# Performance work log

Hardware: AMD Instinct MI355X
Metric: run time of the kernel (lower is better)

Reference implementation:

```python
import jax, jax.numpy as jnp
import numpy as np

IN_F = 4096
OUT_F = 4096
BATCH = 1024

def setup_inputs() -> dict:
    key = jax.random.key(0)
    k = jax.random.split(key, 7)
    x = jax.random.normal(k[0], (BATCH, IN_F), dtype=jnp.float32)
    weight_mu = jax.random.normal(k[1], (OUT_F, IN_F), dtype=jnp.float32) * (1.0 / np.sqrt(IN_F))
    # torch init: uniform(-5,-3) for sigma params (raw values, used directly as std)
    weight_sigma = jax.random.uniform(k[2], (OUT_F, IN_F), dtype=jnp.float32, minval=-5.0, maxval=-3.0)
    bias_mu = jnp.zeros((OUT_F,), dtype=jnp.float32)
    bias_sigma = jax.random.uniform(k[3], (OUT_F,), dtype=jnp.float32, minval=-5.0, maxval=-3.0)
    eps_w = jax.random.normal(k[4], (OUT_F, IN_F), dtype=jnp.float32)
    eps_b = jax.random.normal(k[5], (OUT_F,), dtype=jnp.float32)
    return {"x": x, "weight_mu": weight_mu, "weight_sigma": weight_sigma,
            "bias_mu": bias_mu, "bias_sigma": bias_sigma,
            "eps_w": eps_w, "eps_b": eps_b}

def reference(x, weight_mu, weight_sigma, bias_mu, bias_sigma, eps_w, eps_b):
    # training-mode forward: reparameterized weight sample then dense matmul
    weight = weight_mu + eps_w * weight_sigma        # [out, in]
    bias = bias_mu + eps_b * bias_sigma              # [out]
    # F.linear(x, W, b) = x @ W.T + b
    return jnp.einsum('bi,oi->bo', x, weight) + bias
```

## Files before the change

kernel.cpp:

```cpp
#include <hip/hip_runtime.h>
#include <hip/hip_bf16.h>
#include <stdint.h>

#define M_BATCH 1024
#define N_OUT   4096
#define K_IN    4096

#define BM 128
#define BN 128
#define KPER   (K_IN / 2)
#define BK2    32
#define KITER2 (KPER / BK2)

typedef __attribute__((ext_vector_type(8))) __bf16 bf16x8_t;
typedef __attribute__((ext_vector_type(4))) float f32x4_t;
typedef __attribute__((ext_vector_type(4))) float fvec4;
typedef __attribute__((ext_vector_type(4))) unsigned short us4_t;

__device__ __forceinline__ unsigned short f2bf_bits(float f) {
    union { __hip_bfloat16 h; unsigned short u; } cvt;
    cvt.h = __float2bfloat16(f);
    return cvt.u;
}

__global__ __launch_bounds__(256) void prep_kernel(
    const float* __restrict__ x,
    const float* __restrict__ wmu,
    const float* __restrict__ wsig,
    const float* __restrict__ epsw,
    unsigned short* __restrict__ wb,
    unsigned short* __restrict__ xb)
{
    const size_t tid = (size_t)blockIdx.x * blockDim.x + threadIdx.x;
    const size_t T   = (size_t)1048576;

    const fvec4* wmu4  = (const fvec4*)wmu;
    const fvec4* wsig4 = (const fvec4*)wsig;
    const fvec4* epsw4 = (const fvec4*)epsw;
    us4_t* wb4 = (us4_t*)wb;

    fvec4 m[4], s[4], e[4];
    #pragma unroll
    for (int r = 0; r < 4; ++r) {
        const size_t i = tid + (size_t)r * T;
        m[r] = __builtin_nontemporal_load(wmu4  + i);
        s[r] = __builtin_nontemporal_load(wsig4 + i);
        e[r] = __builtin_nontemporal_load(epsw4 + i);
    }
    #pragma unroll
    for (int r = 0; r < 4; ++r) {
        us4_t o;
        o.x = f2bf_bits(fmaf(e[r].x, s[r].x, m[r].x));
        o.y = f2bf_bits(fmaf(e[r].y, s[r].y, m[r].y));
        o.z = f2bf_bits(fmaf(e[r].z, s[r].z, m[r].z));
        o.w = f2bf_bits(fmaf(e[r].w, s[r].w, m[r].w));
        wb4[tid + (size_t)r * T] = o;
    }

    fvec4 v = __builtin_nontemporal_load((const fvec4*)x + tid);
    us4_t o;
    o.x = f2bf_bits(v.x);
    o.y = f2bf_bits(v.y);
    o.z = f2bf_bits(v.z);
    o.w = f2bf_bits(v.w);
    ((us4_t*)xb)[tid] = o;
}

__global__ __launch_bounds__(512, 2) void gemm_bt_kernel(
    const unsigned short* __restrict__ A,
    const unsigned short* __restrict__ B,
    const float* __restrict__ bmu,
    const float* __restrict__ bsig,
    const float* __restrict__ ebias,
    float* __restrict__ C)
{
    __shared__ unsigned short lds[4 * 16384];

    const int t   = threadIdx.x;
    const int b   = blockIdx.x;
    const int bn  = (b & 7) | (((b >> 3) & 3) << 3);
    const int bm  = b >> 5;
    const int bm0 = bm * BM;
    const int bn0 = bn * BN;
    const int lane  = t & 63;
    const int wave  = t >> 6;
    const int khalf = wave >> 2;
    const int quadw = wave & 3;
    const int wrow  = (quadw >> 1) * 64;
    const int wcol  = (quadw & 1) * 64;
    const int lm    = lane & 15;
    const int quad  = lane >> 4;
    const int fq    = quad ^ ((lm >> 1) & 3);

    f32x4_t acc[4][4] = {};

    const int row   = t >> 2;
    const int chlog = (t & 3) ^ ((t >> 3) & 3);
    const unsigned short* srcs[4];
    srcs[0] = A + (size_t)(bm0 + row) * K_IN + chlog * 8;
    srcs[1] = srcs[0] + KPER;
    srcs[2] = B + (size_t)(bn0 + row) * K_IN + chlog * 8;
    srcs[3] = srcs[2] + KPER;
    char* dstt = (char*)lds + t * 16;

    auto STAGE = [&](int it) {
        const int koff = it * BK2;
        char* d = dstt + (it & 3) * 32768;
        #pragma unroll
        for (int s = 0; s < 4; ++s)
            __builtin_amdgcn_global_load_lds(
                (const __attribute__((address_space(1))) void*)(srcs[s] + koff),
                (__attribute__((address_space(3))) void*)(d + s * 8192), 16, 0, 0);
    };

    auto COMPUTE = [&](int it) {
        const unsigned short* Lb = lds + (it & 3) * 16384;
        const unsigned short* Ah = Lb + khalf * 4096 + (wrow + lm) * 32 + fq * 8;
        const unsigned short* Bh = Lb + 8192 + khalf * 4096 + (wcol + lm) * 32 + fq * 8;
        bf16x8_t a_frag[4], b_frag[4];
        #pragma unroll
        for (int im = 0; im < 4; im++)
            a_frag[im] = *(const bf16x8_t*)(Ah + im * 512);
        #pragma unroll
        for (int jn = 0; jn < 4; jn++)
            b_frag[jn] = *(const bf16x8_t*)(Bh + jn * 512);
        #pragma unroll
        for (int im = 0; im < 4; im++)
            #pragma unroll
            for (int jn = 0; jn < 4; jn++)
                acc[im][jn] = __builtin_amdgcn_mfma_f32_16x16x32_bf16(
                    a_frag[im], b_frag[jn], acc[im][jn], 0, 0, 0);
        __builtin_amdgcn_sched_barrier(0);
    };

    STAGE(0); STAGE(1); STAGE(2);

    for (int it = 0; it < KITER2 - 3; ++it) {
        asm volatile("s_waitcnt vmcnt(8)\n\ts_barrier" ::: "memory");
        STAGE(it + 3);
        COMPUTE(it);
    }
    asm volatile("s_waitcnt vmcnt(8)\n\ts_barrier" ::: "memory");
    COMPUTE(KITER2 - 3);
    asm volatile("s_waitcnt vmcnt(4)\n\ts_barrier" ::: "memory");
    COMPUTE(KITER2 - 2);
    asm volatile("s_waitcnt vmcnt(0)\n\ts_barrier" ::: "memory");
    COMPUTE(KITER2 - 1);

    f32x4_t* red = (f32x4_t*)lds;
    if (wave >= 4) {
        #pragma unroll
        for (int im = 0; im < 4; im++)
            #pragma unroll
            for (int jn = 0; jn < 4; jn++)
                red[quadw * 1024 + (im * 4 + jn) * 64 + lane] = acc[im][jn];
    }
    __syncthreads();
    if (wave < 4) {
        #pragma unroll
        for (int jn = 0; jn < 4; jn++) {
            const int gn = bn0 + wcol + jn * 16 + lm;
            const float bias = bmu[gn] + ebias[gn] * bsig[gn];
            #pragma unroll
            for (int im = 0; im < 4; im++) {
                const f32x4_t part = red[quadw * 1024 + (im * 4 + jn) * 64 + lane];
                const int gm0 = bm0 + wrow + im * 16 + quad * 4;
                #pragma unroll
                for (int r = 0; r < 4; r++)
                    C[(size_t)(gm0 + r) * N_OUT + gn] = acc[im][jn][r] + part[r] + bias;
            }
        }
    }
}

__global__ __launch_bounds__(256) void naive_kernel(
    const float* __restrict__ x, const float* __restrict__ wmu,
    const float* __restrict__ wsig, const float* __restrict__ bmu,
    const float* __restrict__ bsig, const float* __restrict__ epsw,
    const float* __restrict__ epsb, float* __restrict__ out)
{
    const int o = blockIdx.x * blockDim.x + threadIdx.x;
    const int b = blockIdx.y;
    const float4* xr = (const float4*)(x + (size_t)b * K_IN);
    const float4* mr = (const float4*)(wmu + (size_t)o * K_IN);
    const float4* sr = (const float4*)(wsig + (size_t)o * K_IN);
    const float4* er = (const float4*)(epsw + (size_t)o * K_IN);
    float s = 0.f;
    for (int k = 0; k < K_IN / 4; k++) {
        float4 xv = xr[k], m = mr[k], sg = sr[k], e = er[k];
        s += xv.x * fmaf(e.x, sg.x, m.x);
        s += xv.y * fmaf(e.y, sg.y, m.y);
        s += xv.z * fmaf(e.z, sg.z, m.z);
        s += xv.w * fmaf(e.w, sg.w, m.w);
    }
    out[(size_t)b * N_OUT + o] = s + bmu[o] + epsb[o] * bsig[o];
}

extern "C" void kernel_launch(void* const* d_in, const int* in_sizes, int n_in,
                              void* d_out, int out_size, void* d_ws, size_t ws_size,
                              hipStream_t stream)
{
    const float* x    = (const float*)d_in[0];
    const float* wmu  = (const float*)d_in[1];
    const float* wsig = (const float*)d_in[2];
    const float* bmu  = (const float*)d_in[3];
    const float* bsig = (const float*)d_in[4];
    const float* epsw = (const float*)d_in[5];
    const float* epsb = (const float*)d_in[6];
    float* out = (float*)d_out;

    const size_t need = ((size_t)N_OUT * K_IN + (size_t)M_BATCH * K_IN) * sizeof(unsigned short);
    if (ws_size >= need) {
        unsigned short* wb = (unsigned short*)d_ws;
        unsigned short* xb = wb + (size_t)N_OUT * K_IN;
        prep_kernel<<<4096, 256, 0, stream>>>(x, wmu, wsig, epsw, wb, xb);
        gemm_bt_kernel<<<256, 512, 0, stream>>>(xb, wb, bmu, bsig, epsb, out);
    } else {
        dim3 grid(N_OUT / 256, M_BATCH);
        naive_kernel<<<grid, 256, 0, stream>>>(x, wmu, wsig, bmu, bsig, epsw, epsb, out);
    }
}
```

Measured before the change: 246.1 us.

## Fuse weight/activation prep into GEMM with chunked producer flags

```diff
diff --git a/kernel.cpp b/kernel.cpp
--- a/kernel.cpp
+++ b/kernel.cpp
@@ -8,9 +8,11 @@
 
 #define BM 128
 #define BN 128
-#define KPER   (K_IN / 2)
+#define KPER   2048
 #define BK2    32
-#define KITER2 (KPER / BK2)
+#define NSLAB  64
+#define NCHUNK 16
+#define NFLAG  8
 
 typedef __attribute__((ext_vector_type(8))) __bf16 bf16x8_t;
 typedef __attribute__((ext_vector_type(4))) float f32x4_t;
@@ -23,55 +25,17 @@
     return cvt.u;
 }
 
-__global__ __launch_bounds__(256) void prep_kernel(
+__global__ __launch_bounds__(512, 2) void fused_kernel(
     const float* __restrict__ x,
     const float* __restrict__ wmu,
     const float* __restrict__ wsig,
     const float* __restrict__ epsw,
-    unsigned short* __restrict__ wb,
-    unsigned short* __restrict__ xb)
-{
-    const size_t tid = (size_t)blockIdx.x * blockDim.x + threadIdx.x;
-    const size_t T   = (size_t)1048576;
-
-    const fvec4* wmu4  = (const fvec4*)wmu;
-    const fvec4* wsig4 = (const fvec4*)wsig;
-    const fvec4* epsw4 = (const fvec4*)epsw;
-    us4_t* wb4 = (us4_t*)wb;
-
-    fvec4 m[4], s[4], e[4];
-    #pragma unroll
-    for (int r = 0; r < 4; ++r) {
-        const size_t i = tid + (size_t)r * T;
-        m[r] = __builtin_nontemporal_load(wmu4  + i);
-        s[r] = __builtin_nontemporal_load(wsig4 + i);
-        e[r] = __builtin_nontemporal_load(epsw4 + i);
-    }
-    #pragma unroll
-    for (int r = 0; r < 4; ++r) {
-        us4_t o;
-        o.x = f2bf_bits(fmaf(e[r].x, s[r].x, m[r].x));
-        o.y = f2bf_bits(fmaf(e[r].y, s[r].y, m[r].y));
-        o.z = f2bf_bits(fmaf(e[r].z, s[r].z, m[r].z));
-        o.w = f2bf_bits(fmaf(e[r].w, s[r].w, m[r].w));
-        wb4[tid + (size_t)r * T] = o;
-    }
-
-    fvec4 v = __builtin_nontemporal_load((const fvec4*)x + tid);
-    us4_t o;
-    o.x = f2bf_bits(v.x);
-    o.y = f2bf_bits(v.y);
-    o.z = f2bf_bits(v.z);
-    o.w = f2bf_bits(v.w);
-    ((us4_t*)xb)[tid] = o;
-}
-
-__global__ __launch_bounds__(512, 2) void gemm_bt_kernel(
-    const unsigned short* __restrict__ A,
-    const unsigned short* __restrict__ B,
     const float* __restrict__ bmu,
     const float* __restrict__ bsig,
     const float* __restrict__ ebias,
+    unsigned short* __restrict__ wb,
+    unsigned short* __restrict__ xb,
+    unsigned int*   __restrict__ ready,
     float* __restrict__ C)
 {
     __shared__ unsigned short lds[4 * 16384];
@@ -94,27 +58,62 @@
 
     f32x4_t acc[4][4] = {};
 
-    const int row   = t >> 2;
+    const int prow  = b * 16 + (t >> 5);
+    const int pxrow = b * 4 + (t >> 7);
+    fvec4 pm[2], ps[2], pe[2];
+    float px[2];
+
+    auto PRODUCE_LOAD = [&](int cc) {
+        #pragma unroll
+        for (int h = 0; h < 2; ++h) {
+            const size_t wo = (size_t)prow * K_IN + h * KPER + cc * 128 + ((t & 31) << 2);
+            pm[h] = __builtin_nontemporal_load((const fvec4*)(wmu  + wo));
+            ps[h] = __builtin_nontemporal_load((const fvec4*)(wsig + wo));
+            pe[h] = __builtin_nontemporal_load((const fvec4*)(epsw + wo));
+            const size_t xo = (size_t)pxrow * K_IN + h * KPER + cc * 128 + (t & 127);
+            px[h] = __builtin_nontemporal_load(x + xo);
+        }
+    };
+    auto CONVERT_STORE = [&](int cc) {
+        #pragma unroll
+        for (int h = 0; h < 2; ++h) {
+            us4_t o;
+            o.x = f2bf_bits(fmaf(pe[h].x, ps[h].x, pm[h].x));
+            o.y = f2bf_bits(fmaf(pe[h].y, ps[h].y, pm[h].y));
+            o.z = f2bf_bits(fmaf(pe[h].z, ps[h].z, pm[h].z));
+            o.w = f2bf_bits(fmaf(pe[h].w, ps[h].w, pm[h].w));
+            *(us4_t*)(wb + (size_t)prow * K_IN + h * KPER + cc * 128 + ((t & 31) << 2)) = o;
+            xb[(size_t)pxrow * K_IN + h * KPER + cc * 128 + (t & 127)] = f2bf_bits(px[h]);
+        }
+    };
+    auto POLL = [&](int f) {
+        if (t == 0) {
+            while (__hip_atomic_load(&ready[f], __ATOMIC_RELAXED,
+                                     __HIP_MEMORY_SCOPE_AGENT) < 256u)
+                __builtin_amdgcn_s_sleep(2);
+        }
+    };
+
+    const int grow  = t >> 2;
     const int chlog = (t & 3) ^ ((t >> 3) & 3);
     const unsigned short* srcs[4];
-    srcs[0] = A + (size_t)(bm0 + row) * K_IN + chlog * 8;
+    srcs[0] = xb + (size_t)(bm0 + grow) * K_IN + chlog * 8;
     srcs[1] = srcs[0] + KPER;
-    srcs[2] = B + (size_t)(bn0 + row) * K_IN + chlog * 8;
+    srcs[2] = wb + (size_t)(bn0 + grow) * K_IN + chlog * 8;
     srcs[3] = srcs[2] + KPER;
     char* dstt = (char*)lds + t * 16;
 
-    auto STAGE = [&](int it) {
-        const int koff = it * BK2;
-        char* d = dstt + (it & 3) * 32768;
-        #pragma unroll
-        for (int s = 0; s < 4; ++s)
+    auto STAGE = [&](int s) {
+        const int koff = s * BK2;
+        char* d = dstt + (s & 3) * 32768;
+        #pragma unroll
+        for (int q = 0; q < 4; ++q)
             __builtin_amdgcn_global_load_lds(
-                (const __attribute__((address_space(1))) void*)(srcs[s] + koff),
-                (__attribute__((address_space(3))) void*)(d + s * 8192), 16, 0, 0);
-    };
-
-    auto COMPUTE = [&](int it) {
-        const unsigned short* Lb = lds + (it & 3) * 16384;
+                (const __attribute__((address_space(1))) void*)(srcs[q] + koff),
+                (__attribute__((address_space(3))) void*)(d + q * 8192), 16, 0, 0);
+    };
+    auto COMPUTE = [&](int s) {
+        const unsigned short* Lb = lds + (s & 3) * 16384;
         const unsigned short* Ah = Lb + khalf * 4096 + (wrow + lm) * 32 + fq * 8;
         const unsigned short* Bh = Lb + 8192 + khalf * 4096 + (wcol + lm) * 32 + fq * 8;
         bf16x8_t a_frag[4], b_frag[4];
@@ -133,19 +132,59 @@
         __builtin_amdgcn_sched_barrier(0);
     };
 
-    STAGE(0); STAGE(1); STAGE(2);
-
-    for (int it = 0; it < KITER2 - 3; ++it) {
-        asm volatile("s_waitcnt vmcnt(8)\n\ts_barrier" ::: "memory");
-        STAGE(it + 3);
-        COMPUTE(it);
-    }
-    asm volatile("s_waitcnt vmcnt(8)\n\ts_barrier" ::: "memory");
-    COMPUTE(KITER2 - 3);
-    asm volatile("s_waitcnt vmcnt(4)\n\ts_barrier" ::: "memory");
-    COMPUTE(KITER2 - 2);
-    asm volatile("s_waitcnt vmcnt(0)\n\ts_barrier" ::: "memory");
-    COMPUTE(KITER2 - 1);
+    PRODUCE_LOAD(0);
+
+    for (int c = 0; c < 19; ++c) {
+        if (c < NCHUNK) {
+            CONVERT_STORE(c);
+            if (c + 1 < NCHUNK) PRODUCE_LOAD(c + 1);
+        }
+        if (c < 3) {
+            if (c == 1) {
+                asm volatile("s_waitcnt vmcnt(0)" ::: "memory");
+                __builtin_amdgcn_fence(__ATOMIC_RELEASE, "agent");
+                __builtin_amdgcn_s_barrier();
+                if (t == 0)
+                    __hip_atomic_fetch_add(&ready[0], 1u, __ATOMIC_RELAXED,
+                                           __HIP_MEMORY_SCOPE_AGENT);
+            }
+            continue;
+        }
+        const int s0 = (c - 3) * 4;
+        if (c == 3) {
+            POLL(0);
+            __builtin_amdgcn_s_barrier();
+            STAGE(0); STAGE(1); STAGE(2);
+        } else if (c <= 16) {
+            POLL((4 * c - 6) >> 3);
+        }
+        asm volatile("s_waitcnt vmcnt(8)" ::: "memory");
+        __builtin_amdgcn_s_barrier();
+        if (s0 + 3 < NSLAB) STAGE(s0 + 3);
+        COMPUTE(s0 + 0);
+        asm volatile("s_waitcnt vmcnt(8)" ::: "memory");
+        __builtin_amdgcn_s_barrier();
+        if (s0 + 4 < NSLAB) STAGE(s0 + 4);
+        COMPUTE(s0 + 1);
+        const bool sig = (c & 1) && (c <= 15);
+        if (sig) {
+            asm volatile("s_waitcnt vmcnt(0)" ::: "memory");
+            __builtin_amdgcn_fence(__ATOMIC_RELEASE, "agent");
+        }
+        if (c == 18) asm volatile("s_waitcnt vmcnt(4)" ::: "memory");
+        else         asm volatile("s_waitcnt vmcnt(8)" ::: "memory");
+        __builtin_amdgcn_s_barrier();
+        if (sig && t == 0)
+            __hip_atomic_fetch_add(&ready[c >> 1], 1u, __ATOMIC_RELAXED,
+                                   __HIP_MEMORY_SCOPE_AGENT);
+        if (s0 + 5 < NSLAB) STAGE(s0 + 5);
+        COMPUTE(s0 + 2);
+        if (c == 18) asm volatile("s_waitcnt vmcnt(0)" ::: "memory");
+        else         asm volatile("s_waitcnt vmcnt(8)" ::: "memory");
+        __builtin_amdgcn_s_barrier();
+        if (s0 + 6 < NSLAB) STAGE(s0 + 6);
+        COMPUTE(s0 + 3);
+    }
 
     f32x4_t* red = (f32x4_t*)lds;
     if (wave >= 4) {
@@ -209,12 +248,15 @@
     const float* epsb = (const float*)d_in[6];
     float* out = (float*)d_out;
 
-    const size_t need = ((size_t)N_OUT * K_IN + (size_t)M_BATCH * K_IN) * sizeof(unsigned short);
+    const size_t elems = (size_t)N_OUT * K_IN + (size_t)M_BATCH * K_IN;
+    const size_t need  = elems * sizeof(unsigned short) + NFLAG * sizeof(unsigned int);
     if (ws_size >= need) {
         unsigned short* wb = (unsigned short*)d_ws;
         unsigned short* xb = wb + (size_t)N_OUT * K_IN;
-        prep_kernel<<<4096, 256, 0, stream>>>(x, wmu, wsig, epsw, wb, xb);
-        gemm_bt_kernel<<<256, 512, 0, stream>>>(xb, wb, bmu, bsig, epsb, out);
+        unsigned int* ready = (unsigned int*)(xb + (size_t)M_BATCH * K_IN);
+        hipMemsetAsync(ready, 0, NFLAG * sizeof(unsigned int), stream);
+        fused_kernel<<<256, 512, 0, stream>>>(x, wmu, wsig, epsw, bmu, bsig,
+                                              epsb, wb, xb, ready, out);
     } else {
         dim3 grid(N_OUT / 256, M_BATCH);
         naive_kernel<<<grid, 256, 0, stream>>>(x, wmu, wsig, bmu, bsig, epsw, epsb, out);
```

Result: slower. 597.1 us (+142.6%).

## Split GEMM over K into two slices with atomic accumulation and double buffering

Applied to the files above, without the earlier changes.

```diff
diff --git a/kernel.cpp b/kernel.cpp
--- a/kernel.cpp
+++ b/kernel.cpp
@@ -8,9 +8,9 @@
 
 #define BM 128
 #define BN 128
-#define KPER   (K_IN / 2)
-#define BK2    32
-#define KITER2 (KPER / BK2)
+#define KSLICE 2048
+#define BK3    32
+#define KIT3   32
 
 typedef __attribute__((ext_vector_type(8))) __bf16 bf16x8_t;
 typedef __attribute__((ext_vector_type(4))) float f32x4_t;
@@ -66,7 +66,7 @@
     ((us4_t*)xb)[tid] = o;
 }
 
-__global__ __launch_bounds__(512, 2) void gemm_bt_kernel(
+__global__ __launch_bounds__(512, 4) void gemm_splitk_kernel(
     const unsigned short* __restrict__ A,
     const unsigned short* __restrict__ B,
     const float* __restrict__ bmu,
@@ -74,12 +74,13 @@
     const float* __restrict__ ebias,
     float* __restrict__ C)
 {
-    __shared__ unsigned short lds[4 * 16384];
+    __shared__ unsigned short lds[2 * 16384];
 
     const int t   = threadIdx.x;
     const int b   = blockIdx.x;
     const int bn  = (b & 7) | (((b >> 3) & 3) << 3);
-    const int bm  = b >> 5;
+    const int bm  = (b >> 5) & 7;
+    const int ks  = b >> 8;
     const int bm0 = bm * BM;
     const int bn0 = bn * BN;
     const int lane  = t & 63;
@@ -94,27 +95,27 @@
 
     f32x4_t acc[4][4] = {};
 
-    const int row   = t >> 2;
+    const int rlow  = t >> 2;
     const int chlog = (t & 3) ^ ((t >> 3) & 3);
+    const int kb    = ks * KSLICE;
     const unsigned short* srcs[4];
-    srcs[0] = A + (size_t)(bm0 + row) * K_IN + chlog * 8;
-    srcs[1] = srcs[0] + KPER;
-    srcs[2] = B + (size_t)(bn0 + row) * K_IN + chlog * 8;
-    srcs[3] = srcs[2] + KPER;
+    srcs[0] = A + (size_t)(bm0 + rlow) * K_IN + kb + chlog * 8;
+    srcs[1] = srcs[0] + 1024;
+    srcs[2] = B + (size_t)(bn0 + rlow) * K_IN + kb + chlog * 8;
+    srcs[3] = srcs[2] + 1024;
     char* dstt = (char*)lds + t * 16;
 
-    auto STAGE = [&](int it) {
-        const int koff = it * BK2;
-        char* d = dstt + (it & 3) * 32768;
-        #pragma unroll
-        for (int s = 0; s < 4; ++s)
+    auto STAGE = [&](int s) {
+        const int koff = s * BK3;
+        char* d = dstt + (s & 1) * 32768;
+        #pragma unroll
+        for (int q = 0; q < 4; ++q)
             __builtin_amdgcn_global_load_lds(
-                (const __attribute__((address_space(1))) void*)(srcs[s] + koff),
-                (__attribute__((address_space(3))) void*)(d + s * 8192), 16, 0, 0);
+                (const __attribute__((address_space(1))) void*)(srcs[q] + koff),
+                (__attribute__((address_space(3))) void*)(d + q * 8192), 16, 0, 0);
     };
-
-    auto COMPUTE = [&](int it) {
-        const unsigned short* Lb = lds + (it & 3) * 16384;
+    auto COMPUTE = [&](int s) {
+        const unsigned short* Lb = lds + (s & 1) * 16384;
         const unsigned short* Ah = Lb + khalf * 4096 + (wrow + lm) * 32 + fq * 8;
         const unsigned short* Bh = Lb + 8192 + khalf * 4096 + (wcol + lm) * 32 + fq * 8;
         bf16x8_t a_frag[4], b_frag[4];
@@ -133,20 +134,14 @@
         __builtin_amdgcn_sched_barrier(0);
     };
 
-    STAGE(0); STAGE(1); STAGE(2);
-
-    for (int it = 0; it < KITER2 - 3; ++it) {
-        asm volatile("s_waitcnt vmcnt(8)\n\ts_barrier" ::: "memory");
-        STAGE(it + 3);
+    STAGE(0);
+    for (int it = 0; it < KIT3; ++it) {
+        __syncthreads();
+        if (it + 1 < KIT3) STAGE(it + 1);
         COMPUTE(it);
     }
-    asm volatile("s_waitcnt vmcnt(8)\n\ts_barrier" ::: "memory");
-    COMPUTE(KITER2 - 3);
-    asm volatile("s_waitcnt vmcnt(4)\n\ts_barrier" ::: "memory");
-    COMPUTE(KITER2 - 2);
-    asm volatile("s_waitcnt vmcnt(0)\n\ts_barrier" ::: "memory");
-    COMPUTE(KITER2 - 1);
-
+
+    __syncthreads();
     f32x4_t* red = (f32x4_t*)lds;
     if (wave >= 4) {
         #pragma unroll
@@ -160,14 +155,15 @@
         #pragma unroll
         for (int jn = 0; jn < 4; jn++) {
             const int gn = bn0 + wcol + jn * 16 + lm;
-            const float bias = bmu[gn] + ebias[gn] * bsig[gn];
+            const float bias = (ks == 0) ? (bmu[gn] + ebias[gn] * bsig[gn]) : 0.f;
             #pragma unroll
             for (int im = 0; im < 4; im++) {
                 const f32x4_t part = red[quadw * 1024 + (im * 4 + jn) * 64 + lane];
                 const int gm0 = bm0 + wrow + im * 16 + quad * 4;
                 #pragma unroll
                 for (int r = 0; r < 4; r++)
-                    C[(size_t)(gm0 + r) * N_OUT + gn] = acc[im][jn][r] + part[r] + bias;
+                    unsafeAtomicAdd(&C[(size_t)(gm0 + r) * N_OUT + gn],
+                                    acc[im][jn][r] + part[r] + bias);
             }
         }
     }
@@ -213,8 +209,9 @@
     if (ws_size >= need) {
         unsigned short* wb = (unsigned short*)d_ws;
         unsigned short* xb = wb + (size_t)N_OUT * K_IN;
+        hipMemsetAsync(out, 0, (size_t)M_BATCH * N_OUT * sizeof(float), stream);
         prep_kernel<<<4096, 256, 0, stream>>>(x, wmu, wsig, epsw, wb, xb);
-        gemm_bt_kernel<<<256, 512, 0, stream>>>(xb, wb, bmu, bsig, epsb, out);
+        gemm_splitk_kernel<<<512, 512, 0, stream>>>(xb, wb, bmu, bsig, epsb, out);
     } else {
         dim3 grid(N_OUT / 256, M_BATCH);
         naive_kernel<<<grid, 256, 0, stream>>>(x, wmu, wsig, bmu, bsig, epsw, epsb, out);
```

Measured after the change: 270.8 us. 1.1x slower.
